# Kernel tuning notes

Hardware: AMD Instinct MI355X
Metric: run time of the kernel (lower is better)

## Reference

```python
import jax, jax.numpy as jnp
import numpy as np

ENC_DIM, DEC_DIM, JOINT_DIM, VOCAB = 512, 640, 512, 1024
B, T, U = 8, 256, 64


def setup_inputs() -> dict:
    key = jax.random.key(0)
    ks = jax.random.split(key, 8)
    s_enc = 1.0 / np.sqrt(ENC_DIM)
    s_dec = 1.0 / np.sqrt(DEC_DIM)
    s_out = 1.0 / np.sqrt(2 * JOINT_DIM)
    return {
        "enc_out": jax.random.normal(ks[0], (B, T, ENC_DIM), jnp.float32),
        "pred_out": jax.random.normal(ks[1], (B, U, DEC_DIM), jnp.float32),
        "W_enc": jax.random.uniform(ks[2], (JOINT_DIM, ENC_DIM), jnp.float32, -s_enc, s_enc),
        "b_enc": jax.random.uniform(ks[3], (JOINT_DIM,), jnp.float32, -s_enc, s_enc),
        "W_pred": jax.random.uniform(ks[4], (JOINT_DIM, DEC_DIM), jnp.float32, -s_dec, s_dec),
        "b_pred": jax.random.uniform(ks[5], (JOINT_DIM,), jnp.float32, -s_dec, s_dec),
        "W_out": jax.random.uniform(ks[6], (VOCAB, 2 * JOINT_DIM), jnp.float32, -s_out, s_out),
        "b_out": jax.random.uniform(ks[7], (VOCAB,), jnp.float32, -s_out, s_out),
    }


def reference(enc_out, pred_out, W_enc, b_enc, W_pred, b_pred, W_out, b_out):
    # Dropout is identity in eval mode. fc_out on cat([enc_exp, pred_exp]) is
    # mathematically identical to splitting W_out in half and summing two
    # broadcast projections (avoids materializing the [B,T,U,2J] tensor).
    J = W_enc.shape[0]
    e = jnp.einsum('bte,je->btj', enc_out, W_enc) + b_enc    # [B,T,J]
    p = jnp.einsum('bud,jd->buj', pred_out, W_pred) + b_pred  # [B,U,J]
    W1, W2 = W_out[:, :J], W_out[:, J:]
    out = (jnp.einsum('btj,vj->btv', e, W1)[:, :, None, :]
           + jnp.einsum('buj,vj->buv', p, W2)[:, None, :, :]
           + b_out)                                           # [B,T,U,V]
    return out
```

## Files before the change

### kernel.cpp

```cpp
#include <hip/hip_runtime.h>

typedef float f4 __attribute__((ext_vector_type(4)));
typedef float f32x4 __attribute__((ext_vector_type(4)));
typedef short bf16x8 __attribute__((ext_vector_type(8)));
typedef unsigned short u16x8 __attribute__((ext_vector_type(8)));

static __device__ __forceinline__ unsigned short f2bf(float f) {
    unsigned int x = __builtin_bit_cast(unsigned int, f);
    x = (x + 0x7fffu + ((x >> 16) & 1u)) >> 16;
    return (unsigned short)x;
}
static __device__ __forceinline__ float bf2f(unsigned short h) {
    unsigned int x = ((unsigned int)h) << 16;
    return __builtin_bit_cast(float, x);
}

struct CvtJob { const float* src; unsigned short* hi; unsigned short* lo; int n8; };

__global__ __launch_bounds__(256) void convert_kernel(
    CvtJob j0, CvtJob j1, CvtJob j2, CvtJob j3, CvtJob j4, int total8)
{
    CvtJob jobs[5] = { j0, j1, j2, j3, j4 };
    int cum1 = j0.n8, cum2 = cum1 + j1.n8, cum3 = cum2 + j2.n8, cum4 = cum3 + j3.n8;
    for (int g = blockIdx.x * blockDim.x + threadIdx.x; g < total8;
         g += gridDim.x * blockDim.x) {
        int ji, base;
        if      (g < cum1) { ji = 0; base = 0; }
        else if (g < cum2) { ji = 1; base = cum1; }
        else if (g < cum3) { ji = 2; base = cum2; }
        else if (g < cum4) { ji = 3; base = cum3; }
        else               { ji = 4; base = cum4; }
        const CvtJob& J = jobs[ji];
        int idx = (g - base) * 8;
        f4 a = *(const f4*)(J.src + idx);
        f4 b = *(const f4*)(J.src + idx + 4);
        u16x8 hv, lv;
        float s[8] = { a.x, a.y, a.z, a.w, b.x, b.y, b.z, b.w };
        #pragma unroll
        for (int i = 0; i < 8; ++i) {
            unsigned short h = f2bf(s[i]);
            hv[i] = h;
            lv[i] = f2bf(s[i] - bf2f(h));
        }
        *(u16x8*)(J.hi + idx) = hv;
        *(u16x8*)(J.lo + idx) = lv;
    }
}

struct GJob {
    const unsigned short *Ah, *Al, *Wh, *Wl;
    int lda, ldw;
    const float* bias;
    float* Cf;
    unsigned short *Ch, *Cl;
    int N, K, nbx;
};

template<bool SPLIT_OUT>
__global__ __launch_bounds__(256, 2) void gemm64(GJob j0, GJob j1, int nblk0)
{
    __shared__ unsigned short Ah_s[64][40];
    __shared__ unsigned short Al_s[64][40];
    __shared__ unsigned short Wh_s[64][40];
    __shared__ unsigned short Wl_s[64][40];

    const bool first = (int)blockIdx.x < nblk0;
    const GJob J = first ? j0 : j1;
    const int local = first ? (int)blockIdx.x : (int)blockIdx.x - nblk0;
    const int m0 = (local % J.nbx) * 64;
    const int n0 = (local / J.nbx) * 64;

    const int tid  = threadIdx.x;
    const int lane = tid & 63;
    const int wid  = tid >> 6;
    const int wr   = wid >> 1, wc = wid & 1;
    const int row  = tid >> 2, q = (tid & 3) * 8;
    const int lrow = lane & 15, lk = (lane >> 4) * 8;

    const unsigned short* pAh = J.Ah + (size_t)(m0 + row) * J.lda + q;
    const unsigned short* pAl = J.Al + (size_t)(m0 + row) * J.lda + q;
    const unsigned short* pWh = J.Wh + (size_t)(n0 + row) * J.ldw + q;
    const unsigned short* pWl = J.Wl + (size_t)(n0 + row) * J.ldw + q;

    f32x4 acc[2][2];
    #pragma unroll
    for (int i = 0; i < 2; ++i)
        #pragma unroll
        for (int j = 0; j < 2; ++j) acc[i][j] = (f32x4){0.f, 0.f, 0.f, 0.f};

    for (int k0 = 0; k0 < J.K; k0 += 32) {
        u16x8 ra = *(const u16x8*)(pAh + k0);
        u16x8 rb = *(const u16x8*)(pAl + k0);
        u16x8 rc = *(const u16x8*)(pWh + k0);
        u16x8 rd = *(const u16x8*)(pWl + k0);
        if (k0) __syncthreads();
        *(u16x8*)&Ah_s[row][q] = ra;
        *(u16x8*)&Al_s[row][q] = rb;
        *(u16x8*)&Wh_s[row][q] = rc;
        *(u16x8*)&Wl_s[row][q] = rd;
        __syncthreads();

        bf16x8 ah[2], al[2], wh[2], wl[2];
        #pragma unroll
        for (int i = 0; i < 2; ++i) {
            ah[i] = *(const bf16x8*)&Ah_s[wr * 32 + i * 16 + lrow][lk];
            al[i] = *(const bf16x8*)&Al_s[wr * 32 + i * 16 + lrow][lk];
            wh[i] = *(const bf16x8*)&Wh_s[wc * 32 + i * 16 + lrow][lk];
            wl[i] = *(const bf16x8*)&Wl_s[wc * 32 + i * 16 + lrow][lk];
        }
        #pragma unroll
        for (int i = 0; i < 2; ++i)
            #pragma unroll
            for (int j = 0; j < 2; ++j) {
                acc[i][j] = __builtin_amdgcn_mfma_f32_16x16x32_bf16(ah[i], wh[j], acc[i][j], 0, 0, 0);
                acc[i][j] = __builtin_amdgcn_mfma_f32_16x16x32_bf16(ah[i], wl[j], acc[i][j], 0, 0, 0);
                acc[i][j] = __builtin_amdgcn_mfma_f32_16x16x32_bf16(al[i], wh[j], acc[i][j], 0, 0, 0);
            }
    }

    #pragma unroll
    for (int i = 0; i < 2; ++i) {
        const int rbase = m0 + wr * 32 + i * 16 + (lane >> 4) * 4;
        #pragma unroll
        for (int j = 0; j < 2; ++j) {
            const int col = n0 + wc * 32 + j * 16 + (lane & 15);
            const float bv = J.bias ? J.bias[col] : 0.f;
            #pragma unroll
            for (int r = 0; r < 4; ++r) {
                float v = acc[i][j][r] + bv;
                size_t off = (size_t)(rbase + r) * J.N + col;
                if (SPLIT_OUT) {
                    unsigned short h = f2bf(v);
                    J.Ch[off] = h;
                    J.Cl[off] = f2bf(v - bf2f(h));
                } else {
                    J.Cf[off] = v;
                }
            }
        }
    }
}

__global__ __launch_bounds__(256) void bcast_kernel(
    const float* __restrict__ X, const float* __restrict__ Y,
    float* __restrict__ out, int T, int U)
{
    const int Vq  = 256;
    const int bt  = blockIdx.x;
    const int b   = bt / T;
    const int tid = threadIdx.x;

    const f4* X4 = (const f4*)X;
    const f4* Y4 = (const f4*)Y + (size_t)b * U * Vq;
    f4* O4 = (f4*)out + (size_t)bt * U * Vq;

    f4 x = X4[(size_t)bt * Vq + tid];
    #pragma unroll 4
    for (int u = 0; u < U; ++u) {
        f4 y = Y4[u * Vq + tid];
        f4 r = { x.x + y.x, x.y + y.y, x.z + y.z, x.w + y.w };
        __builtin_nontemporal_store(r, &O4[u * Vq + tid]);
    }
}

extern "C" void kernel_launch(void* const* d_in, const int* in_sizes, int n_in,
                              void* d_out, int out_size, void* d_ws, size_t ws_size,
                              hipStream_t stream) {
    (void)in_sizes; (void)n_in; (void)out_size; (void)ws_size;

    const int B = 8, T = 256, U = 64;
    const int ENC = 512, DEC = 640, J = 512, V = 1024;
    const int MT = B * T;
    const int MU = B * U;

    const float* enc    = (const float*)d_in[0];
    const float* pred   = (const float*)d_in[1];
    const float* W_enc  = (const float*)d_in[2];
    const float* b_enc  = (const float*)d_in[3];
    const float* W_pred = (const float*)d_in[4];
    const float* b_pred = (const float*)d_in[5];
    const float* W_out  = (const float*)d_in[6];
    const float* b_out  = (const float*)d_in[7];
    float* out = (float*)d_out;

    const int n_enc  = MT * ENC;
    const int n_pred = MU * DEC;
    const int n_We   = J * ENC;
    const int n_Wp   = J * DEC;
    const int n_Wo   = V * 2 * J;
    const int n_e    = MT * J;
    const int n_p    = MU * J;

    unsigned short* w = (unsigned short*)d_ws;
    unsigned short* enc_h  = w;
    unsigned short* enc_l  = enc_h + n_enc;
    unsigned short* pred_h = enc_l + n_enc;
    unsigned short* pred_l = pred_h + n_pred;
    unsigned short* We_h   = pred_l + n_pred;
    unsigned short* We_l   = We_h + n_We;
    unsigned short* Wp_h   = We_l + n_We;
    unsigned short* Wp_l   = Wp_h + n_Wp;
    unsigned short* Wo_h   = Wp_l + n_Wp;
    unsigned short* Wo_l   = Wo_h + n_Wo;
    unsigned short* e_h    = Wo_l + n_Wo;
    unsigned short* e_l    = e_h + n_e;
    unsigned short* p_h    = e_l + n_e;
    unsigned short* p_l    = p_h + n_p;
    float* ws_X = (float*)(p_l + n_p);
    float* ws_Y = ws_X + (size_t)MT * V;

    CvtJob j0 = { enc,    enc_h,  enc_l,  n_enc  / 8 };
    CvtJob j1 = { pred,   pred_h, pred_l, n_pred / 8 };
    CvtJob j2 = { W_enc,  We_h,   We_l,   n_We   / 8 };
    CvtJob j3 = { W_pred, Wp_h,   Wp_l,   n_Wp   / 8 };
    CvtJob j4 = { W_out,  Wo_h,   Wo_l,   n_Wo   / 8 };
    const int total8 = (n_enc + n_pred + n_We + n_Wp + n_Wo) / 8;
    convert_kernel<<<(total8 + 255) / 256, 256, 0, stream>>>(j0, j1, j2, j3, j4, total8);

    GJob je = { enc_h, enc_l, We_h, We_l, ENC, ENC, b_enc,
                nullptr, e_h, e_l, J, ENC, MT / 64 };
    GJob jp = { pred_h, pred_l, Wp_h, Wp_l, DEC, DEC, b_pred,
                nullptr, p_h, p_l, J, DEC, MU / 64 };
    const int nbe = (MT / 64) * (J / 64);
    const int nbp = (MU / 64) * (J / 64);
    gemm64<true><<<nbe + nbp, 256, 0, stream>>>(je, jp, nbe);

    GJob jx = { e_h, e_l, Wo_h, Wo_l, J, 2 * J, b_out,
                ws_X, nullptr, nullptr, V, J, MT / 64 };
    GJob jy = { p_h, p_l, Wo_h + J, Wo_l + J, J, 2 * J, nullptr,
                ws_Y, nullptr, nullptr, V, J, MU / 64 };
    const int nbx = (MT / 64) * (V / 64);
    const int nby = (MU / 64) * (V / 64);
    gemm64<false><<<nbx + nby, 256, 0, stream>>>(jx, jy, nbx);

    bcast_kernel<<<dim3(B * T), 256, 0, stream>>>(ws_X, ws_Y, out, T, U);
}
```

Measured before the change: 152.8 us.

## Fuse encoder-side output GEMM into broadcast-add kernel

Computes the X = e·W1 + b_out projection inside the broadcast kernel. Each block builds a 16x256 X tile in shared memory with split-bf16 MFMAs, then writes the broadcast sum against Y held in registers. This drops the write and read of the X intermediate through global memory and one kernel launch. The cost is that W1 tiles are reloaded by many small-M blocks, and the GEMM phase now runs ahead of the store-bound broadcast in the same kernel.

```diff
diff --git a/kernel.cpp b/kernel.cpp
--- a/kernel.cpp
+++ b/kernel.cpp
@@ -141,25 +141,104 @@
     }
 }
 
-__global__ __launch_bounds__(256) void bcast_kernel(
-    const float* __restrict__ X, const float* __restrict__ Y,
-    float* __restrict__ out, int T, int U)
+__global__ __launch_bounds__(256, 2) void fused_x_bcast(
+    const unsigned short* __restrict__ eh, const unsigned short* __restrict__ el,
+    const unsigned short* __restrict__ W1h, const unsigned short* __restrict__ W1l,
+    const float* __restrict__ b_out,
+    const float* __restrict__ Y,
+    float* __restrict__ out)
 {
-    const int Vq  = 256;
-    const int bt  = blockIdx.x;
-    const int b   = bt / T;
-    const int tid = threadIdx.x;
-
-    const f4* X4 = (const f4*)X;
-    const f4* Y4 = (const f4*)Y + (size_t)b * U * Vq;
-    f4* O4 = (f4*)out + (size_t)bt * U * Vq;
-
-    f4 x = X4[(size_t)bt * Vq + tid];
-    #pragma unroll 4
-    for (int u = 0; u < U; ++u) {
-        f4 y = Y4[u * Vq + tid];
-        f4 r = { x.x + y.x, x.y + y.y, x.z + y.z, x.w + y.w };
-        __builtin_nontemporal_store(r, &O4[u * Vq + tid]);
+    __shared__ unsigned short Ah_s[16][40];
+    __shared__ unsigned short Al_s[16][40];
+    __shared__ unsigned short Wh_s[256][40];
+    __shared__ unsigned short Wl_s[256][40];
+    __shared__ float Xs[16][260];
+
+    const int tid  = threadIdx.x;
+    const int lane = tid & 63;
+    const int wid  = tid >> 6;
+    const int bt0  = blockIdx.x * 16;
+    const int v0   = blockIdx.y * 256;
+    const int b    = bt0 >> 8;
+    const int lrow = lane & 15, lk = (lane >> 4) * 8;
+    const int ldw  = 1024;
+
+    f32x4 acc[4];
+    #pragma unroll
+    for (int j = 0; j < 4; ++j) acc[j] = (f32x4){0.f, 0.f, 0.f, 0.f};
+
+    for (int k0 = 0; k0 < 512; k0 += 32) {
+        u16x8 w_h[4], w_l[4];
+        #pragma unroll
+        for (int pc = 0; pc < 4; ++pc) {
+            const int c = tid + pc * 256;
+            const int row = c >> 2, q = (c & 3) * 8;
+            w_h[pc] = *(const u16x8*)(W1h + (size_t)(v0 + row) * ldw + k0 + q);
+            w_l[pc] = *(const u16x8*)(W1l + (size_t)(v0 + row) * ldw + k0 + q);
+        }
+        u16x8 a_v = {};
+        if (tid < 128) {
+            const int c = tid & 63;
+            const int row = c >> 2, q = (c & 3) * 8;
+            const unsigned short* src = (tid < 64) ? eh : el;
+            a_v = *(const u16x8*)(src + (size_t)(bt0 + row) * 512 + k0 + q);
+        }
+        if (k0) __syncthreads();
+        #pragma unroll
+        for (int pc = 0; pc < 4; ++pc) {
+            const int c = tid + pc * 256;
+            const int row = c >> 2, q = (c & 3) * 8;
+            *(u16x8*)&Wh_s[row][q] = w_h[pc];
+            *(u16x8*)&Wl_s[row][q] = w_l[pc];
+        }
+        if (tid < 128) {
+            const int c = tid & 63;
+            const int row = c >> 2, q = (c & 3) * 8;
+            if (tid < 64) *(u16x8*)&Ah_s[row][q] = a_v;
+            else          *(u16x8*)&Al_s[row][q] = a_v;
+        }
+        __syncthreads();
+
+        bf16x8 ah = *(const bf16x8*)&Ah_s[lrow][lk];
+        bf16x8 al = *(const bf16x8*)&Al_s[lrow][lk];
+        #pragma unroll
+        for (int j = 0; j < 4; ++j) {
+            bf16x8 wh = *(const bf16x8*)&Wh_s[wid * 64 + j * 16 + lrow][lk];
+            bf16x8 wl = *(const bf16x8*)&Wl_s[wid * 64 + j * 16 + lrow][lk];
+            acc[j] = __builtin_amdgcn_mfma_f32_16x16x32_bf16(ah, wh, acc[j], 0, 0, 0);
+            acc[j] = __builtin_amdgcn_mfma_f32_16x16x32_bf16(ah, wl, acc[j], 0, 0, 0);
+            acc[j] = __builtin_amdgcn_mfma_f32_16x16x32_bf16(al, wh, acc[j], 0, 0, 0);
+        }
+    }
+
+    #pragma unroll
+    for (int j = 0; j < 4; ++j) {
+        const int col = wid * 64 + j * 16 + (lane & 15);
+        const float bv = b_out[v0 + col];
+        #pragma unroll
+        for (int r = 0; r < 4; ++r)
+            Xs[(lane >> 4) * 4 + r][col] = acc[j][r] + bv;
+    }
+    __syncthreads();
+
+    const int vq = tid & 63;
+    const int g  = tid >> 6;
+    const f4* Y4 = (const f4*)Y + (size_t)b * 64 * 256 + v0 / 4 + vq;
+    f4 yreg[16];
+    #pragma unroll
+    for (int uu = 0; uu < 16; ++uu)
+        yreg[uu] = Y4[(size_t)(uu * 4 + g) * 256];
+
+    f4* O4 = (f4*)out + ((size_t)bt0 * 64 + g) * 256 + v0 / 4 + vq;
+    for (int btl = 0; btl < 16; ++btl) {
+        f4 xv = *(const f4*)&Xs[btl][vq * 4];
+        f4* rowp = O4 + (size_t)btl * 64 * 256;
+        #pragma unroll
+        for (int uu = 0; uu < 16; ++uu) {
+            f4 yv = yreg[uu];
+            f4 r = { xv.x + yv.x, xv.y + yv.y, xv.z + yv.z, xv.w + yv.w };
+            __builtin_nontemporal_store(r, &rowp[(size_t)uu * 4 * 256]);
+        }
     }
 }
 
@@ -206,8 +285,7 @@
     unsigned short* e_l    = e_h + n_e;
     unsigned short* p_h    = e_l + n_e;
     unsigned short* p_l    = p_h + n_p;
-    float* ws_X = (float*)(p_l + n_p);
-    float* ws_Y = ws_X + (size_t)MT * V;
+    float* ws_Y = (float*)(p_l + n_p);
 
     CvtJob j0 = { enc,    enc_h,  enc_l,  n_enc  / 8 };
     CvtJob j1 = { pred,   pred_h, pred_l, n_pred / 8 };
@@ -225,13 +303,11 @@
     const int nbp = (MU / 64) * (J / 64);
     gemm64<true><<<nbe + nbp, 256, 0, stream>>>(je, jp, nbe);
 
-    GJob jx = { e_h, e_l, Wo_h, Wo_l, J, 2 * J, b_out,
-                ws_X, nullptr, nullptr, V, J, MT / 64 };
     GJob jy = { p_h, p_l, Wo_h + J, Wo_l + J, J, 2 * J, nullptr,
                 ws_Y, nullptr, nullptr, V, J, MU / 64 };
-    const int nbx = (MT / 64) * (V / 64);
     const int nby = (MU / 64) * (V / 64);
-    gemm64<false><<<nbx + nby, 256, 0, stream>>>(jx, jy, nbx);
-
-    bcast_kernel<<<dim3(B * T), 256, 0, stream>>>(ws_X, ws_Y, out, T, U);
-}
+    gemm64<false><<<nby, 256, 0, stream>>>(jy, jy, nby);
+
+    fused_x_bcast<<<dim3(MT / 16, V / 256), 256, 0, stream>>>(
+        e_h, e_l, Wo_h, Wo_l, b_out, ws_Y, out);
+}
```

Result: slower. 207.4 us (+35.7%).

## Double-buffer GEMM tiles via direct global-to-LDS loads with XOR swizzle

Applied to the files above, without the earlier changes.

Replaces the register-staged global→LDS copy in the split-bf16 GEMM with global_load_lds direct transfers into a double-buffered LDS tile. The next K-slice is prefetched while the MFMAs run on the current one, and the LDS layout is XOR-swizzled in place of padding to avoid bank conflicts. Launch bounds occupancy is raised from 2 to 3. Since a __syncthreads now comes only once per iteration, this relies on the swizzle matching between the writer and reader lanes. It also doubles LDS use per block.

```diff
diff --git a/kernel.cpp b/kernel.cpp
--- a/kernel.cpp
+++ b/kernel.cpp
@@ -13,6 +13,12 @@
 static __device__ __forceinline__ float bf2f(unsigned short h) {
     unsigned int x = ((unsigned int)h) << 16;
     return __builtin_bit_cast(float, x);
+}
+
+static __device__ __forceinline__ void gll16(const unsigned short* g, unsigned short* l) {
+    __builtin_amdgcn_global_load_lds(
+        (__attribute__((address_space(1))) void*)(g),
+        (__attribute__((address_space(3))) void*)(l), 16, 0, 0);
 }
 
 struct CvtJob { const float* src; unsigned short* hi; unsigned short* lo; int n8; };
@@ -56,13 +62,14 @@
     int N, K, nbx;
 };
 
+static __device__ __forceinline__ int fragoff(int r, int s) {
+    return r * 32 + ((s ^ ((r >> 1) & 3)) << 3);
+}
+
 template<bool SPLIT_OUT>
-__global__ __launch_bounds__(256, 2) void gemm64(GJob j0, GJob j1, int nblk0)
+__global__ __launch_bounds__(256, 3) void gemm64(GJob j0, GJob j1, int nblk0)
 {
-    __shared__ unsigned short Ah_s[64][40];
-    __shared__ unsigned short Al_s[64][40];
-    __shared__ unsigned short Wh_s[64][40];
-    __shared__ unsigned short Wl_s[64][40];
+    __shared__ unsigned short lds[2][4][64 * 32];
 
     const bool first = (int)blockIdx.x < nblk0;
     const GJob J = first ? j0 : j1;
@@ -74,13 +81,13 @@
     const int lane = tid & 63;
     const int wid  = tid >> 6;
     const int wr   = wid >> 1, wc = wid & 1;
-    const int row  = tid >> 2, q = (tid & 3) * 8;
-    const int lrow = lane & 15, lk = (lane >> 4) * 8;
-
-    const unsigned short* pAh = J.Ah + (size_t)(m0 + row) * J.lda + q;
-    const unsigned short* pAl = J.Al + (size_t)(m0 + row) * J.lda + q;
-    const unsigned short* pWh = J.Wh + (size_t)(n0 + row) * J.ldw + q;
-    const unsigned short* pWl = J.Wl + (size_t)(n0 + row) * J.ldw + q;
+    const int lrow = lane & 15;
+    const int s    = lane >> 4;
+
+    const int srow  = wid * 16 + (lane >> 2);
+    const int sslot = (lane & 3) ^ ((srow >> 1) & 3);
+    const size_t gA = (size_t)(m0 + srow) * J.lda + sslot * 8;
+    const size_t gW = (size_t)(n0 + srow) * J.ldw + sslot * 8;
 
     f32x4 acc[2][2];
     #pragma unroll
@@ -88,25 +95,34 @@
         #pragma unroll
         for (int j = 0; j < 2; ++j) acc[i][j] = (f32x4){0.f, 0.f, 0.f, 0.f};
 
-    for (int k0 = 0; k0 < J.K; k0 += 32) {
-        u16x8 ra = *(const u16x8*)(pAh + k0);
-        u16x8 rb = *(const u16x8*)(pAl + k0);
-        u16x8 rc = *(const u16x8*)(pWh + k0);
-        u16x8 rd = *(const u16x8*)(pWl + k0);
-        if (k0) __syncthreads();
-        *(u16x8*)&Ah_s[row][q] = ra;
-        *(u16x8*)&Al_s[row][q] = rb;
-        *(u16x8*)&Wh_s[row][q] = rc;
-        *(u16x8*)&Wl_s[row][q] = rd;
-        __syncthreads();
+    const int nt = J.K / 32;
+
+    gll16(J.Ah + gA, &lds[0][0][wid * 512]);
+    gll16(J.Al + gA, &lds[0][1][wid * 512]);
+    gll16(J.Wh + gW, &lds[0][2][wid * 512]);
+    gll16(J.Wl + gW, &lds[0][3][wid * 512]);
+    asm volatile("s_waitcnt vmcnt(0)" ::: "memory");
+    __syncthreads();
+
+    int cur = 0;
+    for (int t = 0; t < nt; ++t) {
+        if (t + 1 < nt) {
+            const int k0 = (t + 1) * 32;
+            gll16(J.Ah + gA + k0, &lds[cur ^ 1][0][wid * 512]);
+            gll16(J.Al + gA + k0, &lds[cur ^ 1][1][wid * 512]);
+            gll16(J.Wh + gW + k0, &lds[cur ^ 1][2][wid * 512]);
+            gll16(J.Wl + gW + k0, &lds[cur ^ 1][3][wid * 512]);
+        }
 
         bf16x8 ah[2], al[2], wh[2], wl[2];
         #pragma unroll
         for (int i = 0; i < 2; ++i) {
-            ah[i] = *(const bf16x8*)&Ah_s[wr * 32 + i * 16 + lrow][lk];
-            al[i] = *(const bf16x8*)&Al_s[wr * 32 + i * 16 + lrow][lk];
-            wh[i] = *(const bf16x8*)&Wh_s[wc * 32 + i * 16 + lrow][lk];
-            wl[i] = *(const bf16x8*)&Wl_s[wc * 32 + i * 16 + lrow][lk];
+            const int ra = wr * 32 + i * 16 + lrow;
+            const int rw = wc * 32 + i * 16 + lrow;
+            ah[i] = *(const bf16x8*)&lds[cur][0][fragoff(ra, s)];
+            al[i] = *(const bf16x8*)&lds[cur][1][fragoff(ra, s)];
+            wh[i] = *(const bf16x8*)&lds[cur][2][fragoff(rw, s)];
+            wl[i] = *(const bf16x8*)&lds[cur][3][fragoff(rw, s)];
         }
         #pragma unroll
         for (int i = 0; i < 2; ++i)
@@ -116,6 +132,12 @@
                 acc[i][j] = __builtin_amdgcn_mfma_f32_16x16x32_bf16(ah[i], wl[j], acc[i][j], 0, 0, 0);
                 acc[i][j] = __builtin_amdgcn_mfma_f32_16x16x32_bf16(al[i], wh[j], acc[i][j], 0, 0, 0);
             }
+
+        if (t + 1 < nt) {
+            asm volatile("s_waitcnt vmcnt(0)" ::: "memory");
+            __syncthreads();
+            cur ^= 1;
+        }
     }
 
     #pragma unroll
```

Result: faster. 145.1 us (-5.0%).
